# Performance work log

Hardware: AMD Instinct MI355X
Metric: run time of the kernel (lower is better)

## Reference

```python
import jax, jax.numpy as jnp
import numpy as np

N = 20000       # nodes
E = 640000      # edges (before self-loops)
F_IN = 128      # num_features
H = 128         # hidden channels (both GAT layers)
C = 40          # num_classes
NEG_SLOPE = 0.2  # PyG GATConv default


def _glorot(key, shape):
    fan = sum(shape)
    return jax.random.normal(key, shape, dtype=jnp.float32) * jnp.sqrt(2.0 / fan)


def setup_inputs() -> dict:
    key = jax.random.key(0)
    ks = jax.random.split(key, 12)
    x = jax.random.normal(ks[0], (N, F_IN), dtype=jnp.float32)
    edge_index = jax.random.randint(ks[1], (2, E), 0, N, dtype=jnp.int64)
    return {
        "x": x,
        "edge_index": edge_index,
        # GATConv layer 1 (heads=1): lin weight, att_src, att_dst, bias
        "W1": _glorot(ks[2], (F_IN, H)),
        "a1_src": _glorot(ks[3], (H,)),
        "a1_dst": _glorot(ks[4], (H,)),
        "b1": jnp.zeros((H,), dtype=jnp.float32),
        # GATConv layer 2
        "W2": _glorot(ks[5], (H, H)),
        "a2_src": _glorot(ks[6], (H,)),
        "a2_dst": _glorot(ks[7], (H,)),
        "b2": jnp.zeros((H,), dtype=jnp.float32),
        # final linear classifier
        "Wl": _glorot(ks[8], (H, C)),
        "bl": jnp.zeros((C,), dtype=jnp.float32),
    }


def gat_conv(x, src, dst, W, a_src, a_dst, b):
    """PyG GATConv, heads=1, concat=True, negative_slope=0.2 (self-loops already in edge list)."""
    h = x @ W                                   # [N, H]
    alpha_src = h @ a_src                       # [N]
    alpha_dst = h @ a_dst                       # [N]
    e = jax.nn.leaky_relu(alpha_src[src] + alpha_dst[dst], NEG_SLOPE)  # [E']
    # numerically stable softmax over incoming edges per destination node
    m = jax.ops.segment_max(e, dst, num_segments=N)        # [N]
    ex = jnp.exp(e - m[dst])                                # [E']
    den = jax.ops.segment_sum(ex, dst, num_segments=N)      # [N]
    alpha = ex / den[dst]                                   # [E']
    out = jax.ops.segment_sum(h[src] * alpha[:, None], dst, num_segments=N)  # [N, H]
    return out + b


def reference(x, edge_index, W1, a1_src, a1_dst, b1, W2, a2_src, a2_dst, b2, Wl, bl):
    # GATConv adds self-loops by default
    loops = jnp.arange(N, dtype=edge_index.dtype)
    src = jnp.concatenate([edge_index[0], loops])
    dst = jnp.concatenate([edge_index[1], loops])
    h = jax.nn.relu(gat_conv(x, src, dst, W1, a1_src, a1_dst, b1))
    h = jax.nn.relu(gat_conv(h, src, dst, W2, a2_src, a2_dst, b2))
    # F.dropout with training=False is identity (eval mode)
    return h @ Wl + bl
```

## Files before the change

### kernel.cpp

```cpp
#include <hip/hip_runtime.h>
#include <hip/hip_fp16.h>
#include <math.h>

#define NNODES 20000
#define NEDGE  640000
#define ETOT   (NEDGE + NNODES)
#define FDIM   128
#define CDIM   40
#define NEG    0.2f

#define NB     157
#define BCAP   6144
#define EPB    2048
#define NBLKA  ((ETOT + EPB - 1) / EPB)

__device__ __forceinline__ float lrelu(float v) { return v >= 0.f ? v : NEG * v; }

__device__ __forceinline__ void edge_sd(const int* __restrict__ ei, int e, int& s, int& d) {
    if (e < NEDGE) { s = ei[e]; d = ei[NEDGE + e]; }
    else { int n = e - NEDGE; s = n; d = n; }
}

__global__ __launch_bounds__(256) void zero_bcnt_k(int* bcnt) {
    if (threadIdx.x < NB) bcnt[threadIdx.x] = 0;
}

__global__ __launch_bounds__(256) void bucketA_k(const int* __restrict__ ei,
                                                 int* __restrict__ bcnt,
                                                 unsigned* __restrict__ bbuf) {
    __shared__ int lhist[NB];
    __shared__ int lbase[NB];
    __shared__ int lcur[NB];
    __shared__ unsigned stash[EPB];
    const int t = threadIdx.x;
    const int e0 = blockIdx.x * EPB;
    for (int i = t; i < NB; i += 256) { lhist[i] = 0; lcur[i] = 0; }
    __syncthreads();
    #pragma unroll
    for (int j = 0; j < EPB / 256; ++j) {
        int e = e0 + j * 256 + t;
        unsigned pk = 0xFFFFFFFFu;
        if (e < ETOT) {
            int s, d; edge_sd(ei, e, s, d);
            atomicAdd(&lhist[d >> 7], 1);
            pk = ((unsigned)(d >> 7) << 22) | ((unsigned)(d & 127) << 15) | (unsigned)s;
        }
        stash[j * 256 + t] = pk;
    }
    __syncthreads();
    for (int i = t; i < NB; i += 256) {
        int c = lhist[i];
        lbase[i] = c ? atomicAdd(&bcnt[i], c) : 0;
    }
    __syncthreads();
    #pragma unroll
    for (int j = 0; j < EPB / 256; ++j) {
        unsigned pk = stash[j * 256 + t];
        if (pk != 0xFFFFFFFFu) {
            int b = pk >> 22;
            int r = atomicAdd(&lcur[b], 1);
            bbuf[(size_t)b * BCAP + lbase[b] + r] = pk & 0x3FFFFFu;
        }
    }
}

__global__ __launch_bounds__(1024) void bucketB_k(const int* __restrict__ bcnt,
                                                  const unsigned* __restrict__ bbuf,
                                                  int* __restrict__ start,
                                                  unsigned* __restrict__ ssd) {
    __shared__ int pre[NB];
    __shared__ int hist[128], hstart[128], hcur[128];
    __shared__ unsigned st[BCAP];
    const int t = threadIdx.x;
    const int b = blockIdx.x;
    if (t < NB) pre[t] = bcnt[t];
    if (t < 128) hist[t] = 0;
    __syncthreads();
    for (int off = 1; off < NB; off <<= 1) {
        int v = 0;
        if (t < NB && t >= off) v = pre[t - off];
        __syncthreads();
        if (t < NB) pre[t] += v;
        __syncthreads();
    }
    const int n0 = bcnt[b];
    const int n = n0 < BCAP ? n0 : BCAP;
    const int base = (b == 0) ? 0 : pre[b - 1];
    for (int i = t; i < n; i += 1024) {
        unsigned pk = bbuf[(size_t)b * BCAP + i];
        st[i] = pk;
        atomicAdd(&hist[(pk >> 15) & 127], 1);
    }
    __syncthreads();
    if (t < 128) hstart[t] = hist[t];
    __syncthreads();
    for (int off = 1; off < 128; off <<= 1) {
        int v = 0;
        if (t < 128 && t >= off) v = hstart[t - off];
        __syncthreads();
        if (t < 128) hstart[t] += v;
        __syncthreads();
    }
    if (t < 128) { int ex = hstart[t] - hist[t]; hstart[t] = ex; hcur[t] = ex; }
    __syncthreads();
    const int d0 = b << 7;
    const int ndst = min(128, NNODES - d0);
    if (t < ndst) start[d0 + t] = base + hstart[t];
    if (b == 0 && t == 0) start[NNODES] = ETOT;
    const unsigned dofs = (unsigned)d0 << 15;
    for (int i = t; i < n; i += 1024) {
        unsigned pk = st[i];
        int r = atomicAdd(&hcur[(pk >> 15) & 127], 1);
        ssd[base + r] = pk + dofs;
    }
}

__global__ __launch_bounds__(256) void edge_p_k(const unsigned* __restrict__ ssd,
                                                const float* __restrict__ asrc,
                                                const float* __restrict__ adst,
                                                float* __restrict__ p) {
    int i = blockIdx.x * 256 + threadIdx.x;
    if (i >= ETOT) return;
    const unsigned v = ssd[i];
    const int s = (int)(v & 0x7FFFu);
    const int d = (int)(v >> 15);
    p[i] = __expf(lrelu(asrc[s] + adst[d]));
}

__global__ __launch_bounds__(256) void gemm_alphas_k(const float* __restrict__ X,
                                                     const float* __restrict__ W,
                                                     const float* __restrict__ a_src,
                                                     const float* __restrict__ a_dst,
                                                     __half* __restrict__ H16,
                                                     float* __restrict__ asrc,
                                                     float* __restrict__ adst) {
    __shared__ float Ws[FDIM * FDIM];
    for (int i = threadIdx.x; i < FDIM * FDIM; i += 256) Ws[i] = W[i];
    __syncthreads();
    const int rsub = threadIdx.x >> 5;
    const int c4 = (threadIdx.x & 31) * 4;
    const int row0 = blockIdx.x * 32 + rsub * 4;
    const float* xr = X + (size_t)row0 * FDIM;
    const float4 as4 = *(const float4*)(a_src + c4);
    const float4 ad4 = *(const float4*)(a_dst + c4);
    float4 acc[4];
    #pragma unroll
    for (int r = 0; r < 4; ++r) acc[r] = make_float4(0.f, 0.f, 0.f, 0.f);
    #pragma unroll 4
    for (int k = 0; k < FDIM; k += 4) {
        const float4 w0 = *(const float4*)(Ws + (k + 0) * FDIM + c4);
        const float4 w1 = *(const float4*)(Ws + (k + 1) * FDIM + c4);
        const float4 w2 = *(const float4*)(Ws + (k + 2) * FDIM + c4);
        const float4 w3 = *(const float4*)(Ws + (k + 3) * FDIM + c4);
        #pragma unroll
        for (int r = 0; r < 4; ++r) {
            const float4 xv = *(const float4*)(xr + (size_t)r * FDIM + k);
            acc[r].x = fmaf(xv.x, w0.x, acc[r].x); acc[r].y = fmaf(xv.x, w0.y, acc[r].y);
            acc[r].z = fmaf(xv.x, w0.z, acc[r].z); acc[r].w = fmaf(xv.x, w0.w, acc[r].w);
            acc[r].x = fmaf(xv.y, w1.x, acc[r].x); acc[r].y = fmaf(xv.y, w1.y, acc[r].y);
            acc[r].z = fmaf(xv.y, w1.z, acc[r].z); acc[r].w = fmaf(xv.y, w1.w, acc[r].w);
            acc[r].x = fmaf(xv.z, w2.x, acc[r].x); acc[r].y = fmaf(xv.z, w2.y, acc[r].y);
            acc[r].z = fmaf(xv.z, w2.z, acc[r].z); acc[r].w = fmaf(xv.z, w2.w, acc[r].w);
            acc[r].x = fmaf(xv.w, w3.x, acc[r].x); acc[r].y = fmaf(xv.w, w3.y, acc[r].y);
            acc[r].z = fmaf(xv.w, w3.z, acc[r].z); acc[r].w = fmaf(xv.w, w3.w, acc[r].w);
        }
    }
    #pragma unroll
    for (int r = 0; r < 4; ++r) {
        union { __half2 h[2]; float2 f; } u;
        u.h[0] = __floats2half2_rn(acc[r].x, acc[r].y);
        u.h[1] = __floats2half2_rn(acc[r].z, acc[r].w);
        *(float2*)(H16 + (size_t)(row0 + r) * FDIM + c4) = u.f;
        float ps = acc[r].x * as4.x + acc[r].y * as4.y + acc[r].z * as4.z + acc[r].w * as4.w;
        float pd = acc[r].x * ad4.x + acc[r].y * ad4.y + acc[r].z * ad4.z + acc[r].w * ad4.w;
        #pragma unroll
        for (int off = 16; off; off >>= 1) {
            ps += __shfl_down(ps, off, 32);
            pd += __shfl_down(pd, off, 32);
        }
        if ((threadIdx.x & 31) == 0) { asrc[row0 + r] = ps; adst[row0 + r] = pd; }
    }
}

__global__ __launch_bounds__(256) void gat_agg_k(const __half* __restrict__ H16,
                                                 const float* __restrict__ p,
                                                 const unsigned* __restrict__ ssd,
                                                 const int* __restrict__ start,
                                                 const float* __restrict__ bias,
                                                 float* __restrict__ out) {
    int w = (blockIdx.x * 256 + threadIdx.x) >> 6;
    if (w >= NNODES) return;
    const int lane = threadIdx.x & 63;
    const int lo = start[w], hi = start[w + 1];
    const size_t coff = (size_t)lane * 2;
    float den = 0.f, a0 = 0.f, a1 = 0.f;
    int i = lo;
    for (; i + 16 <= hi; i += 16) {
        int s[16]; float pp[16];
        #pragma unroll
        for (int j = 0; j < 16; ++j) {
            s[j] = (int)(ssd[i + j] & 0x7FFFu);
            pp[j] = p[i + j];
        }
        __half2 hv[16];
        #pragma unroll
        for (int j = 0; j < 16; ++j)
            hv[j] = *(const __half2*)(H16 + (size_t)s[j] * FDIM + coff);
        #pragma unroll
        for (int j = 0; j < 16; ++j) {
            const float2 f = __half22float2(hv[j]);
            den += pp[j];
            a0 = fmaf(pp[j], f.x, a0);
            a1 = fmaf(pp[j], f.y, a1);
        }
    }
    for (; i + 4 <= hi; i += 4) {
        int s[4]; float pp[4];
        #pragma unroll
        for (int j = 0; j < 4; ++j) {
            s[j] = (int)(ssd[i + j] & 0x7FFFu);
            pp[j] = p[i + j];
        }
        __half2 hv[4];
        #pragma unroll
        for (int j = 0; j < 4; ++j)
            hv[j] = *(const __half2*)(H16 + (size_t)s[j] * FDIM + coff);
        #pragma unroll
        for (int j = 0; j < 4; ++j) {
            const float2 f = __half22float2(hv[j]);
            den += pp[j];
            a0 = fmaf(pp[j], f.x, a0);
            a1 = fmaf(pp[j], f.y, a1);
        }
    }
    for (; i < hi; ++i) {
        const int s = (int)(ssd[i] & 0x7FFFu);
        const float pj = p[i];
        const float2 f = __half22float2(*(const __half2*)(H16 + (size_t)s * FDIM + coff));
        den += pj;
        a0 = fmaf(pj, f.x, a0);
        a1 = fmaf(pj, f.y, a1);
    }
    const float inv = 1.f / den;
    const float v0 = fmaf(a0, inv, bias[lane * 2]);
    const float v1 = fmaf(a1, inv, bias[lane * 2 + 1]);
    float* o = out + (size_t)w * FDIM + coff;
    o[0] = v0 > 0.f ? v0 : 0.f;
    o[1] = v1 > 0.f ? v1 : 0.f;
}

__global__ __launch_bounds__(320) void classifier_k(const float* __restrict__ H,
                                                    const float* __restrict__ Wl,
                                                    const float* __restrict__ bl,
                                                    float* __restrict__ out) {
    __shared__ float Ws[FDIM * CDIM];
    __shared__ float bs[CDIM];
    for (int i = threadIdx.x; i < FDIM * CDIM; i += 320) Ws[i] = Wl[i];
    if (threadIdx.x < CDIM) bs[threadIdx.x] = bl[threadIdx.x];
    __syncthreads();
    const int cq = threadIdx.x % 10;
    const int rsub = threadIdx.x / 10;
    const int c4 = cq * 4;
    const int row0 = blockIdx.x * 64 + rsub * 2;
    const int r0 = min(row0, NNODES - 1);
    const int r1 = min(row0 + 1, NNODES - 1);
    const float* x0 = H + (size_t)r0 * FDIM;
    const float* x1 = H + (size_t)r1 * FDIM;
    float4 a0 = make_float4(0.f, 0.f, 0.f, 0.f);
    float4 a1 = make_float4(0.f, 0.f, 0.f, 0.f);
    #pragma unroll 4
    for (int k = 0; k < FDIM; k += 4) {
        const float4 w0 = *(const float4*)(Ws + (k + 0) * CDIM + c4);
        const float4 w1 = *(const float4*)(Ws + (k + 1) * CDIM + c4);
        const float4 w2 = *(const float4*)(Ws + (k + 2) * CDIM + c4);
        const float4 w3 = *(const float4*)(Ws + (k + 3) * CDIM + c4);
        const float4 v0 = *(const float4*)(x0 + k);
        const float4 v1 = *(const float4*)(x1 + k);
        a0.x = fmaf(v0.x, w0.x, a0.x); a0.y = fmaf(v0.x, w0.y, a0.y);
        a0.z = fmaf(v0.x, w0.z, a0.z); a0.w = fmaf(v0.x, w0.w, a0.w);
        a0.x = fmaf(v0.y, w1.x, a0.x); a0.y = fmaf(v0.y, w1.y, a0.y);
        a0.z = fmaf(v0.y, w1.z, a0.z); a0.w = fmaf(v0.y, w1.w, a0.w);
        a0.x = fmaf(v0.z, w2.x, a0.x); a0.y = fmaf(v0.z, w2.y, a0.y);
        a0.z = fmaf(v0.z, w2.z, a0.z); a0.w = fmaf(v0.z, w2.w, a0.w);
        a0.x = fmaf(v0.w, w3.x, a0.x); a0.y = fmaf(v0.w, w3.y, a0.y);
        a0.z = fmaf(v0.w, w3.z, a0.z); a0.w = fmaf(v0.w, w3.w, a0.w);
        a1.x = fmaf(v1.x, w0.x, a1.x); a1.y = fmaf(v1.x, w0.y, a1.y);
        a1.z = fmaf(v1.x, w0.z, a1.z); a1.w = fmaf(v1.x, w0.w, a1.w);
        a1.x = fmaf(v1.y, w1.x, a1.x); a1.y = fmaf(v1.y, w1.y, a1.y);
        a1.z = fmaf(v1.y, w1.z, a1.z); a1.w = fmaf(v1.y, w1.w, a1.w);
        a1.x = fmaf(v1.z, w2.x, a1.x); a1.y = fmaf(v1.z, w2.y, a1.y);
        a1.z = fmaf(v1.z, w2.z, a1.z); a1.w = fmaf(v1.z, w2.w, a1.w);
        a1.x = fmaf(v1.w, w3.x, a1.x); a1.y = fmaf(v1.w, w3.y, a1.y);
        a1.z = fmaf(v1.w, w3.z, a1.z); a1.w = fmaf(v1.w, w3.w, a1.w);
    }
    const float4 bb = *(const float4*)(bs + c4);
    a0.x += bb.x; a0.y += bb.y; a0.z += bb.z; a0.w += bb.w;
    a1.x += bb.x; a1.y += bb.y; a1.z += bb.z; a1.w += bb.w;
    if (row0 < NNODES)     *(float4*)(out + (size_t)row0 * CDIM + c4) = a0;
    if (row0 + 1 < NNODES) *(float4*)(out + (size_t)(row0 + 1) * CDIM + c4) = a1;
}

extern "C" void kernel_launch(void* const* d_in, const int* in_sizes, int n_in,
                              void* d_out, int out_size, void* d_ws, size_t ws_size,
                              hipStream_t stream) {
    const float* x   = (const float*)d_in[0];
    const int*   ei  = (const int*)d_in[1];
    const float* W1  = (const float*)d_in[2];
    const float* a1s = (const float*)d_in[3];
    const float* a1d = (const float*)d_in[4];
    const float* b1  = (const float*)d_in[5];
    const float* W2  = (const float*)d_in[6];
    const float* a2s = (const float*)d_in[7];
    const float* a2d = (const float*)d_in[8];
    const float* b2  = (const float*)d_in[9];
    const float* Wl  = (const float*)d_in[10];
    const float* bl  = (const float*)d_in[11];
    float* out = (float*)d_out;

    char* ws = (char*)d_ws;
    __half*   H16   = (__half*)(ws);
    float*    bufB  = (float*)(ws + 5120000);
    float*    asrc  = (float*)(ws + 15360000);
    float*    adst  = (float*)(ws + 15440000);
    int*      start = (int*)  (ws + 15520000);
    unsigned* ssd   = (unsigned*)(ws + 15600004);
    int*      bcnt  = (int*)  (ws + 18240004);
    unsigned* bbuf  = (unsigned*)(ws + 18240632);
    float*    pbuf  = (float*)bbuf;

    const int gEdge = (ETOT + 255) / 256;

    zero_bcnt_k<<<1, 256, 0, stream>>>(bcnt);
    bucketA_k<<<NBLKA, 256, 0, stream>>>(ei, bcnt, bbuf);
    bucketB_k<<<NB, 1024, 0, stream>>>(bcnt, bbuf, start, ssd);

    gemm_alphas_k<<<625, 256, 0, stream>>>(x, W1, a1s, a1d, H16, asrc, adst);
    edge_p_k<<<gEdge, 256, 0, stream>>>(ssd, asrc, adst, pbuf);
    gat_agg_k<<<5000, 256, 0, stream>>>(H16, pbuf, ssd, start, b1, bufB);

    gemm_alphas_k<<<625, 256, 0, stream>>>(bufB, W2, a2s, a2d, H16, asrc, adst);
    edge_p_k<<<gEdge, 256, 0, stream>>>(ssd, asrc, adst, pbuf);
    gat_agg_k<<<5000, 256, 0, stream>>>(H16, pbuf, ssd, start, b2, bufB);

    classifier_k<<<313, 320, 0, stream>>>(bufB, Wl, bl, out);
}
```

Baseline: 139.0 us.

## Split fp16 feature table into column halves and aggregate each half separately

The GEMM now writes the fp16 node features as two column-half tables of 64 channels each. Aggregation runs in two passes, each gathering one half, so the gathered working set is 2.56 MB per pass and may fit better in cache. Loads of edge indices and weights use nontemporal hints, and the output uses nontemporal stores. In exchange, the index and p arrays are read twice, two extra launches are added, and each lane loads only 2-byte elements.

```diff
diff --git a/kernel.cpp b/kernel.cpp
--- a/kernel.cpp
+++ b/kernel.cpp
@@ -8,6 +8,7 @@
 #define FDIM   128
 #define CDIM   40
 #define NEG    0.2f
+#define HHALF  (NNODES * 64)
 
 #define NB     157
 #define BCAP   6144
@@ -131,7 +132,7 @@
                                                      const float* __restrict__ W,
                                                      const float* __restrict__ a_src,
                                                      const float* __restrict__ a_dst,
-                                                     __half* __restrict__ H16,
+                                                     __half* __restrict__ Hbase,
                                                      float* __restrict__ asrc,
                                                      float* __restrict__ adst) {
     __shared__ float Ws[FDIM * FDIM];
@@ -165,12 +166,14 @@
             acc[r].z = fmaf(xv.w, w3.z, acc[r].z); acc[r].w = fmaf(xv.w, w3.w, acc[r].w);
         }
     }
+    __half* hdst = Hbase + (c4 < 64 ? (size_t)0 : (size_t)HHALF) ;
+    const int ch = c4 & 63;
     #pragma unroll
     for (int r = 0; r < 4; ++r) {
         union { __half2 h[2]; float2 f; } u;
         u.h[0] = __floats2half2_rn(acc[r].x, acc[r].y);
         u.h[1] = __floats2half2_rn(acc[r].z, acc[r].w);
-        *(float2*)(H16 + (size_t)(row0 + r) * FDIM + c4) = u.f;
+        *(float2*)(hdst + (size_t)(row0 + r) * 64 + ch) = u.f;
         float ps = acc[r].x * as4.x + acc[r].y * as4.y + acc[r].z * as4.z + acc[r].w * as4.w;
         float pd = acc[r].x * ad4.x + acc[r].y * ad4.y + acc[r].z * ad4.z + acc[r].w * ad4.w;
         #pragma unroll
@@ -182,71 +185,67 @@
     }
 }
 
-__global__ __launch_bounds__(256) void gat_agg_k(const __half* __restrict__ H16,
-                                                 const float* __restrict__ p,
-                                                 const unsigned* __restrict__ ssd,
-                                                 const int* __restrict__ start,
-                                                 const float* __restrict__ bias,
-                                                 float* __restrict__ out) {
+__global__ __launch_bounds__(256) void gat_agg_half_k(const __half* __restrict__ Hh,
+                                                      const float* __restrict__ p,
+                                                      const unsigned* __restrict__ ssd,
+                                                      const int* __restrict__ start,
+                                                      const float* __restrict__ bias,
+                                                      float* __restrict__ out,
+                                                      int colbase) {
     int w = (blockIdx.x * 256 + threadIdx.x) >> 6;
     if (w >= NNODES) return;
     const int lane = threadIdx.x & 63;
+    const unsigned short* Hu = (const unsigned short*)Hh;
     const int lo = start[w], hi = start[w + 1];
-    const size_t coff = (size_t)lane * 2;
-    float den = 0.f, a0 = 0.f, a1 = 0.f;
+    float den = 0.f, a = 0.f;
     int i = lo;
     for (; i + 16 <= hi; i += 16) {
         int s[16]; float pp[16];
         #pragma unroll
         for (int j = 0; j < 16; ++j) {
-            s[j] = (int)(ssd[i + j] & 0x7FFFu);
-            pp[j] = p[i + j];
-        }
-        __half2 hv[16];
+            s[j] = (int)(__builtin_nontemporal_load(&ssd[i + j]) & 0x7FFFu);
+            pp[j] = __builtin_nontemporal_load(&p[i + j]);
+        }
+        unsigned short hv[16];
         #pragma unroll
         for (int j = 0; j < 16; ++j)
-            hv[j] = *(const __half2*)(H16 + (size_t)s[j] * FDIM + coff);
+            hv[j] = Hu[(size_t)s[j] * 64 + lane];
         #pragma unroll
         for (int j = 0; j < 16; ++j) {
-            const float2 f = __half22float2(hv[j]);
+            union { unsigned short u; __half h; } c; c.u = hv[j];
             den += pp[j];
-            a0 = fmaf(pp[j], f.x, a0);
-            a1 = fmaf(pp[j], f.y, a1);
+            a = fmaf(pp[j], __half2float(c.h), a);
         }
     }
     for (; i + 4 <= hi; i += 4) {
         int s[4]; float pp[4];
         #pragma unroll
         for (int j = 0; j < 4; ++j) {
-            s[j] = (int)(ssd[i + j] & 0x7FFFu);
-            pp[j] = p[i + j];
-        }
-        __half2 hv[4];
+            s[j] = (int)(__builtin_nontemporal_load(&ssd[i + j]) & 0x7FFFu);
+            pp[j] = __builtin_nontemporal_load(&p[i + j]);
+        }
+        unsigned short hv[4];
         #pragma unroll
         for (int j = 0; j < 4; ++j)
-            hv[j] = *(const __half2*)(H16 + (size_t)s[j] * FDIM + coff);
+            hv[j] = Hu[(size_t)s[j] * 64 + lane];
         #pragma unroll
         for (int j = 0; j < 4; ++j) {
-            const float2 f = __half22float2(hv[j]);
+            union { unsigned short u; __half h; } c; c.u = hv[j];
             den += pp[j];
-            a0 = fmaf(pp[j], f.x, a0);
-            a1 = fmaf(pp[j], f.y, a1);
+            a = fmaf(pp[j], __half2float(c.h), a);
         }
     }
     for (; i < hi; ++i) {
-        const int s = (int)(ssd[i] & 0x7FFFu);
-        const float pj = p[i];
-        const float2 f = __half22float2(*(const __half2*)(H16 + (size_t)s * FDIM + coff));
+        const int s = (int)(__builtin_nontemporal_load(&ssd[i]) & 0x7FFFu);
+        const float pj = __builtin_nontemporal_load(&p[i]);
+        union { unsigned short u; __half h; } c; c.u = Hu[(size_t)s * 64 + lane];
         den += pj;
-        a0 = fmaf(pj, f.x, a0);
-        a1 = fmaf(pj, f.y, a1);
+        a = fmaf(pj, __half2float(c.h), a);
     }
     const float inv = 1.f / den;
-    const float v0 = fmaf(a0, inv, bias[lane * 2]);
-    const float v1 = fmaf(a1, inv, bias[lane * 2 + 1]);
-    float* o = out + (size_t)w * FDIM + coff;
-    o[0] = v0 > 0.f ? v0 : 0.f;
-    o[1] = v1 > 0.f ? v1 : 0.f;
+    float v = fmaf(a, inv, bias[colbase + lane]);
+    v = v > 0.f ? v : 0.f;
+    __builtin_nontemporal_store(v, out + (size_t)w * FDIM + colbase + lane);
 }
 
 __global__ __launch_bounds__(320) void classifier_k(const float* __restrict__ H,
@@ -328,6 +327,9 @@
     unsigned* bbuf  = (unsigned*)(ws + 18240632);
     float*    pbuf  = (float*)bbuf;
 
+    __half* Hlo = H16;
+    __half* Hhi = H16 + HHALF;
+
     const int gEdge = (ETOT + 255) / 256;
 
     zero_bcnt_k<<<1, 256, 0, stream>>>(bcnt);
@@ -336,11 +338,13 @@
 
     gemm_alphas_k<<<625, 256, 0, stream>>>(x, W1, a1s, a1d, H16, asrc, adst);
     edge_p_k<<<gEdge, 256, 0, stream>>>(ssd, asrc, adst, pbuf);
-    gat_agg_k<<<5000, 256, 0, stream>>>(H16, pbuf, ssd, start, b1, bufB);
+    gat_agg_half_k<<<5000, 256, 0, stream>>>(Hlo, pbuf, ssd, start, b1, bufB, 0);
+    gat_agg_half_k<<<5000, 256, 0, stream>>>(Hhi, pbuf, ssd, start, b1, bufB, 64);
 
     gemm_alphas_k<<<625, 256, 0, stream>>>(bufB, W2, a2s, a2d, H16, asrc, adst);
     edge_p_k<<<gEdge, 256, 0, stream>>>(ssd, asrc, adst, pbuf);
-    gat_agg_k<<<5000, 256, 0, stream>>>(H16, pbuf, ssd, start, b2, bufB);
+    gat_agg_half_k<<<5000, 256, 0, stream>>>(Hlo, pbuf, ssd, start, b2, bufB, 0);
+    gat_agg_half_k<<<5000, 256, 0, stream>>>(Hhi, pbuf, ssd, start, b2, bufB, 64);
 
     classifier_k<<<313, 320, 0, stream>>>(bufB, Wl, bl, out);
 }
```

Result: slower. 193.4 us (+39.1%).

## Split each node's edge range across two waves and store aggregation output in fp16

Applied to the files above, without the earlier changes.

The aggregation kernel now handles two nodes per block, and each node's incoming edge range is split between two wavefronts. The partial sums and denominators are combined through shared memory, which adds more parallelism for the latency-bound gather. The aggregated hidden state is also written as fp16, and the layer-2 GEMM and the classifier read fp16 inputs, halving that intermediate traffic. The cost is a block-level sync, an inner unroll reduced from 16 to 8, and extra rounding error from storing activations in half precision.

```diff
diff --git a/kernel.cpp b/kernel.cpp
--- a/kernel.cpp
+++ b/kernel.cpp
@@ -127,13 +127,13 @@
     p[i] = __expf(lrelu(asrc[s] + adst[d]));
 }
 
-__global__ __launch_bounds__(256) void gemm_alphas_k(const float* __restrict__ X,
-                                                     const float* __restrict__ W,
-                                                     const float* __restrict__ a_src,
-                                                     const float* __restrict__ a_dst,
-                                                     __half* __restrict__ H16,
-                                                     float* __restrict__ asrc,
-                                                     float* __restrict__ adst) {
+__global__ __launch_bounds__(256) void gemm_alphas_f32_k(const float* __restrict__ X,
+                                                         const float* __restrict__ W,
+                                                         const float* __restrict__ a_src,
+                                                         const float* __restrict__ a_dst,
+                                                         __half* __restrict__ H16,
+                                                         float* __restrict__ asrc,
+                                                         float* __restrict__ adst) {
     __shared__ float Ws[FDIM * FDIM];
     for (int i = threadIdx.x; i < FDIM * FDIM; i += 256) Ws[i] = W[i];
     __syncthreads();
@@ -182,74 +182,126 @@
     }
 }
 
+__global__ __launch_bounds__(256) void gemm_alphas_f16_k(const __half* __restrict__ X,
+                                                         const float* __restrict__ W,
+                                                         const float* __restrict__ a_src,
+                                                         const float* __restrict__ a_dst,
+                                                         __half* __restrict__ H16,
+                                                         float* __restrict__ asrc,
+                                                         float* __restrict__ adst) {
+    __shared__ float Ws[FDIM * FDIM];
+    for (int i = threadIdx.x; i < FDIM * FDIM; i += 256) Ws[i] = W[i];
+    __syncthreads();
+    const int rsub = threadIdx.x >> 5;
+    const int c4 = (threadIdx.x & 31) * 4;
+    const int row0 = blockIdx.x * 32 + rsub * 4;
+    const __half* xr = X + (size_t)row0 * FDIM;
+    const float4 as4 = *(const float4*)(a_src + c4);
+    const float4 ad4 = *(const float4*)(a_dst + c4);
+    float4 acc[4];
+    #pragma unroll
+    for (int r = 0; r < 4; ++r) acc[r] = make_float4(0.f, 0.f, 0.f, 0.f);
+    #pragma unroll 4
+    for (int k = 0; k < FDIM; k += 4) {
+        const float4 w0 = *(const float4*)(Ws + (k + 0) * FDIM + c4);
+        const float4 w1 = *(const float4*)(Ws + (k + 1) * FDIM + c4);
+        const float4 w2 = *(const float4*)(Ws + (k + 2) * FDIM + c4);
+        const float4 w3 = *(const float4*)(Ws + (k + 3) * FDIM + c4);
+        #pragma unroll
+        for (int r = 0; r < 4; ++r) {
+            union { float2 f2; __half2 h2[2]; } ux;
+            ux.f2 = *(const float2*)(xr + (size_t)r * FDIM + k);
+            const float2 xlo = __half22float2(ux.h2[0]);
+            const float2 xhi = __half22float2(ux.h2[1]);
+            acc[r].x = fmaf(xlo.x, w0.x, acc[r].x); acc[r].y = fmaf(xlo.x, w0.y, acc[r].y);
+            acc[r].z = fmaf(xlo.x, w0.z, acc[r].z); acc[r].w = fmaf(xlo.x, w0.w, acc[r].w);
+            acc[r].x = fmaf(xlo.y, w1.x, acc[r].x); acc[r].y = fmaf(xlo.y, w1.y, acc[r].y);
+            acc[r].z = fmaf(xlo.y, w1.z, acc[r].z); acc[r].w = fmaf(xlo.y, w1.w, acc[r].w);
+            acc[r].x = fmaf(xhi.x, w2.x, acc[r].x); acc[r].y = fmaf(xhi.x, w2.y, acc[r].y);
+            acc[r].z = fmaf(xhi.x, w2.z, acc[r].z); acc[r].w = fmaf(xhi.x, w2.w, acc[r].w);
+            acc[r].x = fmaf(xhi.y, w3.x, acc[r].x); acc[r].y = fmaf(xhi.y, w3.y, acc[r].y);
+            acc[r].z = fmaf(xhi.y, w3.z, acc[r].z); acc[r].w = fmaf(xhi.y, w3.w, acc[r].w);
+        }
+    }
+    #pragma unroll
+    for (int r = 0; r < 4; ++r) {
+        union { __half2 h[2]; float2 f; } u;
+        u.h[0] = __floats2half2_rn(acc[r].x, acc[r].y);
+        u.h[1] = __floats2half2_rn(acc[r].z, acc[r].w);
+        *(float2*)(H16 + (size_t)(row0 + r) * FDIM + c4) = u.f;
+        float ps = acc[r].x * as4.x + acc[r].y * as4.y + acc[r].z * as4.z + acc[r].w * as4.w;
+        float pd = acc[r].x * ad4.x + acc[r].y * ad4.y + acc[r].z * ad4.z + acc[r].w * ad4.w;
+        #pragma unroll
+        for (int off = 16; off; off >>= 1) {
+            ps += __shfl_down(ps, off, 32);
+            pd += __shfl_down(pd, off, 32);
+        }
+        if ((threadIdx.x & 31) == 0) { asrc[row0 + r] = ps; adst[row0 + r] = pd; }
+    }
+}
+
 __global__ __launch_bounds__(256) void gat_agg_k(const __half* __restrict__ H16,
                                                  const float* __restrict__ p,
                                                  const unsigned* __restrict__ ssd,
                                                  const int* __restrict__ start,
                                                  const float* __restrict__ bias,
-                                                 float* __restrict__ out) {
-    int w = (blockIdx.x * 256 + threadIdx.x) >> 6;
-    if (w >= NNODES) return;
+                                                 __half* __restrict__ out16) {
+    __shared__ float sden[4];
+    __shared__ float sacc[4][128];
+    const int wv = threadIdx.x >> 6;
     const int lane = threadIdx.x & 63;
-    const int lo = start[w], hi = start[w + 1];
+    const int w = blockIdx.x * 2 + (wv >> 1);
+    const int part = wv & 1;
+    float den = 0.f, a0 = 0.f, a1 = 0.f;
     const size_t coff = (size_t)lane * 2;
-    float den = 0.f, a0 = 0.f, a1 = 0.f;
-    int i = lo;
-    for (; i + 16 <= hi; i += 16) {
-        int s[16]; float pp[16];
-        #pragma unroll
-        for (int j = 0; j < 16; ++j) {
-            s[j] = (int)(ssd[i + j] & 0x7FFFu);
-            pp[j] = p[i + j];
-        }
-        __half2 hv[16];
-        #pragma unroll
-        for (int j = 0; j < 16; ++j)
-            hv[j] = *(const __half2*)(H16 + (size_t)s[j] * FDIM + coff);
-        #pragma unroll
-        for (int j = 0; j < 16; ++j) {
-            const float2 f = __half22float2(hv[j]);
-            den += pp[j];
-            a0 = fmaf(pp[j], f.x, a0);
-            a1 = fmaf(pp[j], f.y, a1);
-        }
-    }
-    for (; i + 4 <= hi; i += 4) {
-        int s[4]; float pp[4];
-        #pragma unroll
-        for (int j = 0; j < 4; ++j) {
-            s[j] = (int)(ssd[i + j] & 0x7FFFu);
-            pp[j] = p[i + j];
-        }
-        __half2 hv[4];
-        #pragma unroll
-        for (int j = 0; j < 4; ++j)
-            hv[j] = *(const __half2*)(H16 + (size_t)s[j] * FDIM + coff);
-        #pragma unroll
-        for (int j = 0; j < 4; ++j) {
-            const float2 f = __half22float2(hv[j]);
-            den += pp[j];
-            a0 = fmaf(pp[j], f.x, a0);
-            a1 = fmaf(pp[j], f.y, a1);
-        }
-    }
-    for (; i < hi; ++i) {
-        const int s = (int)(ssd[i] & 0x7FFFu);
-        const float pj = p[i];
-        const float2 f = __half22float2(*(const __half2*)(H16 + (size_t)s * FDIM + coff));
-        den += pj;
-        a0 = fmaf(pj, f.x, a0);
-        a1 = fmaf(pj, f.y, a1);
-    }
-    const float inv = 1.f / den;
-    const float v0 = fmaf(a0, inv, bias[lane * 2]);
-    const float v1 = fmaf(a1, inv, bias[lane * 2 + 1]);
-    float* o = out + (size_t)w * FDIM + coff;
-    o[0] = v0 > 0.f ? v0 : 0.f;
-    o[1] = v1 > 0.f ? v1 : 0.f;
-}
-
-__global__ __launch_bounds__(320) void classifier_k(const float* __restrict__ H,
+    if (w < NNODES) {
+        const int lo0 = start[w], hi0 = start[w + 1];
+        const int mid = (lo0 + hi0 + 1) >> 1;
+        int i = part ? mid : lo0;
+        const int hi = part ? hi0 : mid;
+        for (; i + 8 <= hi; i += 8) {
+            int s[8]; float pp[8];
+            #pragma unroll
+            for (int j = 0; j < 8; ++j) {
+                s[j] = (int)(ssd[i + j] & 0x7FFFu);
+                pp[j] = p[i + j];
+            }
+            __half2 hv[8];
+            #pragma unroll
+            for (int j = 0; j < 8; ++j)
+                hv[j] = *(const __half2*)(H16 + (size_t)s[j] * FDIM + coff);
+            #pragma unroll
+            for (int j = 0; j < 8; ++j) {
+                const float2 f = __half22float2(hv[j]);
+                den += pp[j];
+                a0 = fmaf(pp[j], f.x, a0);
+                a1 = fmaf(pp[j], f.y, a1);
+            }
+        }
+        for (; i < hi; ++i) {
+            const int s = (int)(ssd[i] & 0x7FFFu);
+            const float pj = p[i];
+            const float2 f = __half22float2(*(const __half2*)(H16 + (size_t)s * FDIM + coff));
+            den += pj;
+            a0 = fmaf(pj, f.x, a0);
+            a1 = fmaf(pj, f.y, a1);
+        }
+    }
+    sacc[wv][lane * 2] = a0;
+    sacc[wv][lane * 2 + 1] = a1;
+    if (lane == 0) sden[wv] = den;
+    __syncthreads();
+    if (part == 0 && w < NNODES) {
+        const float inv = 1.f / (sden[wv] + sden[wv + 1]);
+        float v0 = fmaf(sacc[wv][lane * 2] + sacc[wv + 1][lane * 2], inv, bias[lane * 2]);
+        float v1 = fmaf(sacc[wv][lane * 2 + 1] + sacc[wv + 1][lane * 2 + 1], inv, bias[lane * 2 + 1]);
+        v0 = v0 > 0.f ? v0 : 0.f;
+        v1 = v1 > 0.f ? v1 : 0.f;
+        *(__half2*)(out16 + (size_t)w * FDIM + coff) = __floats2half2_rn(v0, v1);
+    }
+}
+
+__global__ __launch_bounds__(320) void classifier_k(const __half* __restrict__ H,
                                                     const float* __restrict__ Wl,
                                                     const float* __restrict__ bl,
                                                     float* __restrict__ out) {
@@ -264,8 +316,8 @@
     const int row0 = blockIdx.x * 64 + rsub * 2;
     const int r0 = min(row0, NNODES - 1);
     const int r1 = min(row0 + 1, NNODES - 1);
-    const float* x0 = H + (size_t)r0 * FDIM;
-    const float* x1 = H + (size_t)r1 * FDIM;
+    const __half* x0 = H + (size_t)r0 * FDIM;
+    const __half* x1 = H + (size_t)r1 * FDIM;
     float4 a0 = make_float4(0.f, 0.f, 0.f, 0.f);
     float4 a1 = make_float4(0.f, 0.f, 0.f, 0.f);
     #pragma unroll 4
@@ -274,24 +326,29 @@
         const float4 w1 = *(const float4*)(Ws + (k + 1) * CDIM + c4);
         const float4 w2 = *(const float4*)(Ws + (k + 2) * CDIM + c4);
         const float4 w3 = *(const float4*)(Ws + (k + 3) * CDIM + c4);
-        const float4 v0 = *(const float4*)(x0 + k);
-        const float4 v1 = *(const float4*)(x1 + k);
-        a0.x = fmaf(v0.x, w0.x, a0.x); a0.y = fmaf(v0.x, w0.y, a0.y);
-        a0.z = fmaf(v0.x, w0.z, a0.z); a0.w = fmaf(v0.x, w0.w, a0.w);
-        a0.x = fmaf(v0.y, w1.x, a0.x); a0.y = fmaf(v0.y, w1.y, a0.y);
-        a0.z = fmaf(v0.y, w1.z, a0.z); a0.w = fmaf(v0.y, w1.w, a0.w);
-        a0.x = fmaf(v0.z, w2.x, a0.x); a0.y = fmaf(v0.z, w2.y, a0.y);
-        a0.z = fmaf(v0.z, w2.z, a0.z); a0.w = fmaf(v0.z, w2.w, a0.w);
-        a0.x = fmaf(v0.w, w3.x, a0.x); a0.y = fmaf(v0.w, w3.y, a0.y);
-        a0.z = fmaf(v0.w, w3.z, a0.z); a0.w = fmaf(v0.w, w3.w, a0.w);
-        a1.x = fmaf(v1.x, w0.x, a1.x); a1.y = fmaf(v1.x, w0.y, a1.y);
-        a1.z = fmaf(v1.x, w0.z, a1.z); a1.w = fmaf(v1.x, w0.w, a1.w);
-        a1.x = fmaf(v1.y, w1.x, a1.x); a1.y = fmaf(v1.y, w1.y, a1.y);
-        a1.z = fmaf(v1.y, w1.z, a1.z); a1.w = fmaf(v1.y, w1.w, a1.w);
-        a1.x = fmaf(v1.z, w2.x, a1.x); a1.y = fmaf(v1.z, w2.y, a1.y);
-        a1.z = fmaf(v1.z, w2.z, a1.z); a1.w = fmaf(v1.z, w2.w, a1.w);
-        a1.x = fmaf(v1.w, w3.x, a1.x); a1.y = fmaf(v1.w, w3.y, a1.y);
-        a1.z = fmaf(v1.w, w3.z, a1.z); a1.w = fmaf(v1.w, w3.w, a1.w);
+        union { float2 f2; __half2 h2[2]; } u0, u1;
+        u0.f2 = *(const float2*)(x0 + k);
+        u1.f2 = *(const float2*)(x1 + k);
+        const float2 v0lo = __half22float2(u0.h2[0]);
+        const float2 v0hi = __half22float2(u0.h2[1]);
+        const float2 v1lo = __half22float2(u1.h2[0]);
+        const float2 v1hi = __half22float2(u1.h2[1]);
+        a0.x = fmaf(v0lo.x, w0.x, a0.x); a0.y = fmaf(v0lo.x, w0.y, a0.y);
+        a0.z = fmaf(v0lo.x, w0.z, a0.z); a0.w = fmaf(v0lo.x, w0.w, a0.w);
+        a0.x = fmaf(v0lo.y, w1.x, a0.x); a0.y = fmaf(v0lo.y, w1.y, a0.y);
+        a0.z = fmaf(v0lo.y, w1.z, a0.z); a0.w = fmaf(v0lo.y, w1.w, a0.w);
+        a0.x = fmaf(v0hi.x, w2.x, a0.x); a0.y = fmaf(v0hi.x, w2.y, a0.y);
+        a0.z = fmaf(v0hi.x, w2.z, a0.z); a0.w = fmaf(v0hi.x, w2.w, a0.w);
+        a0.x = fmaf(v0hi.y, w3.x, a0.x); a0.y = fmaf(v0hi.y, w3.y, a0.y);
+        a0.z = fmaf(v0hi.y, w3.z, a0.z); a0.w = fmaf(v0hi.y, w3.w, a0.w);
+        a1.x = fmaf(v1lo.x, w0.x, a1.x); a1.y = fmaf(v1lo.x, w0.y, a1.y);
+        a1.z = fmaf(v1lo.x, w0.z, a1.z); a1.w = fmaf(v1lo.x, w0.w, a1.w);
+        a1.x = fmaf(v1lo.y, w1.x, a1.x); a1.y = fmaf(v1lo.y, w1.y, a1.y);
+        a1.z = fmaf(v1lo.y, w1.z, a1.z); a1.w = fmaf(v1lo.y, w1.w, a1.w);
+        a1.x = fmaf(v1hi.x, w2.x, a1.x); a1.y = fmaf(v1hi.x, w2.y, a1.y);
+        a1.z = fmaf(v1hi.x, w2.z, a1.z); a1.w = fmaf(v1hi.x, w2.w, a1.w);
+        a1.x = fmaf(v1hi.y, w3.x, a1.x); a1.y = fmaf(v1hi.y, w3.y, a1.y);
+        a1.z = fmaf(v1hi.y, w3.z, a1.z); a1.w = fmaf(v1hi.y, w3.w, a1.w);
     }
     const float4 bb = *(const float4*)(bs + c4);
     a0.x += bb.x; a0.y += bb.y; a0.z += bb.z; a0.w += bb.w;
@@ -318,8 +375,8 @@
     float* out = (float*)d_out;
 
     char* ws = (char*)d_ws;
-    __half*   H16   = (__half*)(ws);
-    float*    bufB  = (float*)(ws + 5120000);
+    __half*   bufH  = (__half*)(ws);
+    __half*   bufO  = (__half*)(ws + 5120000);
     float*    asrc  = (float*)(ws + 15360000);
     float*    adst  = (float*)(ws + 15440000);
     int*      start = (int*)  (ws + 15520000);
@@ -329,18 +386,19 @@
     float*    pbuf  = (float*)bbuf;
 
     const int gEdge = (ETOT + 255) / 256;
+    const int gAgg  = (NNODES + 1) / 2;
 
     zero_bcnt_k<<<1, 256, 0, stream>>>(bcnt);
     bucketA_k<<<NBLKA, 256, 0, stream>>>(ei, bcnt, bbuf);
     bucketB_k<<<NB, 1024, 0, stream>>>(bcnt, bbuf, start, ssd);
 
-    gemm_alphas_k<<<625, 256, 0, stream>>>(x, W1, a1s, a1d, H16, asrc, adst);
+    gemm_alphas_f32_k<<<625, 256, 0, stream>>>(x, W1, a1s, a1d, bufH, asrc, adst);
     edge_p_k<<<gEdge, 256, 0, stream>>>(ssd, asrc, adst, pbuf);
-    gat_agg_k<<<5000, 256, 0, stream>>>(H16, pbuf, ssd, start, b1, bufB);
-
-    gemm_alphas_k<<<625, 256, 0, stream>>>(bufB, W2, a2s, a2d, H16, asrc, adst);
+    gat_agg_k<<<gAgg, 256, 0, stream>>>(bufH, pbuf, ssd, start, b1, bufO);
+
+    gemm_alphas_f16_k<<<625, 256, 0, stream>>>(bufO, W2, a2s, a2d, bufH, asrc, adst);
     edge_p_k<<<gEdge, 256, 0, stream>>>(ssd, asrc, adst, pbuf);
-    gat_agg_k<<<5000, 256, 0, stream>>>(H16, pbuf, ssd, start, b2, bufB);
-
-    classifier_k<<<313, 320, 0, stream>>>(bufB, Wl, bl, out);
-}
+    gat_agg_k<<<gAgg, 256, 0, stream>>>(bufH, pbuf, ssd, start, b2, bufO);
+
+    classifier_k<<<313, 320, 0, stream>>>(bufO, Wl, bl, out);
+}
```

New measurement: 155.4 us. 11.8% more time.
